# Performance work log

Hardware: AMD Instinct MI355X
Metric: run time of the kernel (lower is better)

Reference implementation:

```python
import jax, jax.numpy as jnp
import numpy as np
import math

N, E, H, NB, NL, NG, NELEM = 50000, 800000, 64, 8, 2, 64, 100
CUTOFF = 5.0


def _lin(k, fin, fout):
    kw, kb = jax.random.split(k)
    bound = 1.0 / math.sqrt(fin)
    w = jax.random.uniform(kw, (fin, fout), jnp.float32, -bound, bound)
    b = jax.random.uniform(kb, (fout,), jnp.float32, -bound, bound)
    return w, b


def setup_inputs() -> dict:
    key = jax.random.key(0)
    ks = jax.random.split(key, 12)
    z = jax.random.randint(ks[0], (N,), 0, NELEM)
    pos = jax.random.normal(ks[1], (N, 3), jnp.float32)
    edge_index = jax.random.randint(ks[2], (2, E), 0, N)
    batch = jnp.sort(jax.random.randint(ks[3], (N,), 0, NG))
    embed = jax.random.normal(ks[4], (NELEM, H), jnp.float32)
    # stacked per-interaction MLP params, leading dim = NL
    msg_w1, msg_b1, msg_w2, msg_b2 = [], [], [], []
    upd_w1, upd_b1, upd_w2, upd_b2 = [], [], [], []
    for l in range(NL):
        kl = jax.random.fold_in(ks[5], l)
        k1, k2, k3, k4 = jax.random.split(kl, 4)
        w, b = _lin(k1, 2 * H + NB, H); msg_w1.append(w); msg_b1.append(b)
        w, b = _lin(k2, H, H); msg_w2.append(w); msg_b2.append(b)
        w, b = _lin(k3, 2 * H, H); upd_w1.append(w); upd_b1.append(b)
        w, b = _lin(k4, H, H); upd_w2.append(w); upd_b2.append(b)
    eh_w1, eh_b1 = _lin(ks[6], H, H)
    eh_w2, eh_b2 = _lin(ks[7], H, 1)
    return {
        "z": z, "pos": pos, "edge_index": edge_index, "batch": batch,
        "embed": embed,
        "msg_w1": jnp.stack(msg_w1), "msg_b1": jnp.stack(msg_b1),
        "msg_w2": jnp.stack(msg_w2), "msg_b2": jnp.stack(msg_b2),
        "upd_w1": jnp.stack(upd_w1), "upd_b1": jnp.stack(upd_b1),
        "upd_w2": jnp.stack(upd_w2), "upd_b2": jnp.stack(upd_b2),
        "eh_w1": eh_w1, "eh_b1": eh_b1, "eh_w2": eh_w2, "eh_b2": eh_b2,
    }


def _mace_energy(pos, embed, msg_w1, msg_b1, msg_w2, msg_b2,
                 upd_w1, upd_b1, upd_w2, upd_b2,
                 eh_w1, eh_b1, eh_w2, eh_b2,
                 z, edge_index, batch):
    row, col = edge_index[0], edge_index[1]
    edge_vec = pos[row] - pos[col]                      # (E,3)
    d = jnp.linalg.norm(edge_vec, axis=-1)              # (E,)
    env = jnp.where(d < CUTOFF,
                    jnp.cos(d * (math.pi / (2 * CUTOFF))) ** 2,
                    0.0)
    freqs = jnp.arange(1, NB + 1, dtype=pos.dtype) * (math.pi / CUTOFF)
    d_safe = jnp.where(d > 0, d, 1.0)[:, None]
    edge_attr = jnp.sin(freqs * d[:, None]) / d_safe * env[:, None]  # (E,NB)

    x = embed[z]                                        # (N,H)
    for l in range(NL):
        # PyG source_to_target: x_j = x[row], x_i = x[col], aggregate at col
        msg_in = jnp.concatenate([x[col], x[row], edge_attr], axis=-1)  # (E,2H+NB)
        m = jax.nn.silu(msg_in @ msg_w1[l] + msg_b1[l]) @ msg_w2[l] + msg_b2[l]
        agg = jax.ops.segment_sum(m, col, num_segments=N)               # (N,H)
        u_in = jnp.concatenate([x, agg], axis=-1)
        upd = jax.nn.silu(u_in @ upd_w1[l] + upd_b1[l]) @ upd_w2[l] + upd_b2[l]
        x = x + upd

    atomic_e = jax.nn.silu(x @ eh_w1 + eh_b1) @ eh_w2 + eh_b2           # (N,1)
    energy = jax.ops.segment_sum(atomic_e, batch, num_segments=NG)      # (NG,1)
    return energy.squeeze(-1)


def reference(z, pos, edge_index, batch, embed,
              msg_w1, msg_b1, msg_w2, msg_b2,
              upd_w1, upd_b1, upd_w2, upd_b2,
              eh_w1, eh_b1, eh_w2, eh_b2):
    return _mace_energy(pos, embed, msg_w1, msg_b1, msg_w2, msg_b2,
                        upd_w1, upd_b1, upd_w2, upd_b2,
                        eh_w1, eh_b1, eh_w2, eh_b2,
                        z, edge_index, batch)
```

## Files before the change

### kernel.cpp

```cpp
#include <hip/hip_runtime.h>
#include <math.h>

#define NN 50000
#define EE 800000
#define HH 64
#define NBASIS 8
#define NLAYER 2
#define NGRAPH 64
#define NBLK1 49

using half2_t = decltype(__builtin_amdgcn_cvt_pkrtz(0.0f, 0.0f));
typedef _Float16 f16x8 __attribute__((ext_vector_type(8)));
typedef float f32x4 __attribute__((ext_vector_type(4)));

union U4H8 { uint4 u; f16x8 h; };

__device__ __forceinline__ float silu_f(float v) {
    return v * (1.0f / (1.0f + __expf(-v)));
}

__device__ __forceinline__ unsigned pk2(float a, float b) {
    union { half2_t h; unsigned u; } x;
    x.h = __builtin_amdgcn_cvt_pkrtz(a, b);
    return x.u;
}

__device__ __forceinline__ half2_t u2h(unsigned u) {
    union { unsigned u; half2_t h; } x; x.u = u; return x.h;
}

__global__ __launch_bounds__(256) void prep_k(
    const int* __restrict__ z, const float* __restrict__ embed,
    unsigned* __restrict__ xh,
    const float* __restrict__ msg_w1, const float* __restrict__ msg_w2,
    const float* __restrict__ upd_w1, const float* __restrict__ upd_w2,
    const float* __restrict__ eh_w1,
    unsigned* __restrict__ w1t, unsigned* __restrict__ w2t,
    unsigned* __restrict__ w1tu, unsigned* __restrict__ w2tu,
    unsigned* __restrict__ ehw1t,
    const int* __restrict__ ecol, int* __restrict__ deg)
{
    int b = blockIdx.x;
    if (b < 6250) {
        int idx = b * 256 + threadIdx.x;
        int n = idx >> 5;
        int p = idx & 31;
        const float2* er = (const float2*)(embed + ((size_t)z[n] << 6));
        float2 v = er[p];
        xh[idx] = pk2(v.x, v.y);
    } else if (b < 6362) {
        int idx = (b - 6250) * 256 + threadIdx.x;
        if (idx < 10240) {
            int l = idx / 5120, rem = idx % 5120;
            int f = rem / 80, kp = rem % 80;
            const float* w = msg_w1 + (size_t)l * 136 * 64;
            unsigned v = 0;
            if (kp < 68) v = pk2(w[(2*kp)*64 + f], w[(2*kp+1)*64 + f]);
            w1t[idx] = v;
        } else if (idx < 14336) {
            int j = idx - 10240;
            int l = j / 2048, rem = j % 2048;
            int n = rem / 32, kp = rem % 32;
            const float* w = msg_w2 + (size_t)l * 64 * 64;
            w2t[j] = pk2(w[(2*kp)*64 + n], w[(2*kp+1)*64 + n]);
        } else if (idx < 22528) {
            int j = idx - 14336;
            int l = j / 4096, rem = j % 4096;
            int f = rem >> 6, kp = rem & 63;
            const float* w = upd_w1 + (size_t)l * 128 * 64;
            w1tu[j] = pk2(w[(2*kp)*64 + f], w[(2*kp+1)*64 + f]);
        } else if (idx < 26624) {
            int j = idx - 22528;
            int l = j / 2048, rem = j % 2048;
            int n = rem / 32, kp = rem % 32;
            const float* w = upd_w2 + (size_t)l * 64 * 64;
            w2tu[j] = pk2(w[(2*kp)*64 + n], w[(2*kp+1)*64 + n]);
        } else if (idx < 28672) {
            int j = idx - 26624;
            int f = j / 32, kp = j % 32;
            ehw1t[j] = pk2(eh_w1[(2*kp)*64 + f], eh_w1[(2*kp+1)*64 + f]);
        }
    } else {
        int e = (b - 6362) * 256 + threadIdx.x;
        if (e < EE) atomicAdd(&deg[ecol[e]], 1);
    }
}

__global__ __launch_bounds__(1024) void scan1_k(
    const int* __restrict__ deg, int* __restrict__ cursor,
    int* __restrict__ bsum)
{
    __shared__ int wsum[16];
    int t = threadIdx.x, lane = t & 63, wave = t >> 6;
    int i = blockIdx.x * 1024 + t;
    int v = (i < NN) ? deg[i] : 0;
    int s = v;
#pragma unroll
    for (int off = 1; off < 64; off <<= 1) {
        int tv = __shfl_up(s, off, 64);
        if (lane >= off) s += tv;
    }
    if (lane == 63) wsum[wave] = s;
    __syncthreads();
    if (wave == 0) {
        int ws = (lane < 16) ? wsum[lane] : 0;
        int ss = ws;
#pragma unroll
        for (int off = 1; off < 16; off <<= 1) {
            int tv = __shfl_up(ss, off, 64);
            if (lane >= off) ss += tv;
        }
        if (lane < 16) wsum[lane] = ss - ws;
    }
    __syncthreads();
    int excl = wsum[wave] + s - v;
    if (i < NN) cursor[i] = excl;
    if (t == 1023) bsum[blockIdx.x] = excl + v;
}

__global__ __launch_bounds__(64) void scan2_k(int* __restrict__ bsum)
{
    int lane = threadIdx.x;
    int v = (lane < NBLK1) ? bsum[lane] : 0;
    int s = v;
#pragma unroll
    for (int off = 1; off < 64; off <<= 1) {
        int tv = __shfl_up(s, off, 64);
        if (lane >= off) s += tv;
    }
    if (lane < NBLK1) bsum[lane] = s - v;
}

__global__ __launch_bounds__(256) void scatter_k(
    const int* __restrict__ erow, const int* __restrict__ ecol,
    const float* __restrict__ pos,
    int* __restrict__ cursor, const int* __restrict__ bsum,
    uint4* __restrict__ edgeS)
{
    int e = blockIdx.x * 256 + threadIdx.x;
    if (e >= EE) return;
    int c = ecol[e], r = erow[e];
    int slot = atomicAdd(&cursor[c], 1) + bsum[c >> 10];
    float dx = pos[3*r]   - pos[3*c];
    float dy = pos[3*r+1] - pos[3*c+1];
    float dz = pos[3*r+2] - pos[3*c+2];
    float d = sqrtf(dx*dx + dy*dy + dz*dz);
    uint4 v;
    v.x = (unsigned)r; v.y = (unsigned)c;
    v.z = __float_as_uint(d); v.w = 0;
    edgeS[slot] = v;
}

__global__ __launch_bounds__(256, 4) void msg_k(
    const uint4* __restrict__ edgeS,
    const unsigned* __restrict__ xh,
    const unsigned* __restrict__ w1t, const float* __restrict__ b1,
    const unsigned* __restrict__ w2t, const float* __restrict__ b2,
    float* __restrict__ agg)
{
    __shared__ __align__(16) unsigned earr[4][64 * 4];
    __shared__ int ckey_s[4][64];
    __shared__ int rkey_s[4][64];
    __shared__ float Mbuf[4][64 * 33];

    const int wid  = threadIdx.x >> 6;
    const int lane = threadIdx.x & 63;
    const int q = lane >> 4, n15 = lane & 15;
    const size_t base = (size_t)blockIdx.x * 256 + wid * 64;

    int mykey;
    {
        uint4 ev = edgeS[base + lane];
        rkey_s[wid][lane] = (int)ev.x;
        mykey = (int)ev.y;
        ckey_s[wid][lane] = mykey;
        float d = __uint_as_float(ev.z);
        float env = 0.0f;
        if (d < 5.0f) {
            float cv = __cosf(d * 0.31415926535897932f);
            env = cv * cv;
        }
        float scale = (d > 0.0f) ? (env / d) : env;
        float ea[NBASIS];
#pragma unroll
        for (int k = 0; k < NBASIS; ++k)
            ea[k] = __sinf((float)(k + 1) * 0.62831853071795865f * d) * scale;
#pragma unroll
        for (int p = 0; p < 4; ++p)
            earr[wid][lane * 4 + p] = pk2(ea[2*p], ea[2*p+1]);
    }
    int pkk = __shfl_up(mykey, 1, 64);
    unsigned long long bmask = __ballot(lane > 0 && mykey != pkk);
    unsigned m32 = (unsigned)(bmask >> (lane & 32));
    __syncthreads();

    int cn[4], rn[4];
#pragma unroll
    for (int nt = 0; nt < 4; ++nt) {
        int eB = nt * 16 + n15;
        cn[nt] = ckey_s[wid][eB];
        rn[nt] = rkey_s[wid][eB];
    }

    f32x4 acc1[4][4];
#pragma unroll
    for (int mt = 0; mt < 4; ++mt) {
        f32x4 binit = *(const f32x4*)(b1 + mt * 16 + q * 4);
#pragma unroll
        for (int nt = 0; nt < 4; ++nt) acc1[mt][nt] = binit;
    }
#pragma unroll
    for (int ks = 0; ks < 5; ++ks) {
        U4H8 bfk[4];
#pragma unroll
        for (int nt = 0; nt < 4; ++nt) {
            if (ks == 4) {
                uint4 zz; zz.x = zz.y = zz.z = zz.w = 0;
                bfk[nt].u = (q == 0) ? *(const uint4*)(earr[wid] + (nt * 16 + n15) * 4) : zz;
            } else if (ks < 2) {
                bfk[nt].u = ((const uint4*)(xh + ((size_t)cn[nt] << 5)))[ks * 4 + q];
            } else {
                bfk[nt].u = ((const uint4*)(xh + ((size_t)rn[nt] << 5)))[(ks - 2) * 4 + q];
            }
        }
#pragma unroll
        for (int mt = 0; mt < 4; ++mt) {
            U4H8 af;
            af.u = *(const uint4*)(w1t + (size_t)(mt * 16 + n15) * 80 + ks * 16 + q * 4);
#pragma unroll
            for (int nt = 0; nt < 4; ++nt)
                acc1[mt][nt] = __builtin_amdgcn_mfma_f32_16x16x32_f16(
                    af.h, bfk[nt].h, acc1[mt][nt], 0, 0, 0);
        }
    }

    unsigned psrc[4][4][2];
#pragma unroll
    for (int mt = 0; mt < 4; ++mt)
#pragma unroll
        for (int nt = 0; nt < 4; ++nt) {
            psrc[mt][nt][0] = pk2(silu_f(acc1[mt][nt][0]), silu_f(acc1[mt][nt][1]));
            psrc[mt][nt][1] = pk2(silu_f(acc1[mt][nt][2]), silu_f(acc1[mt][nt][3]));
        }

    f32x4 acc2[4][4];
#pragma unroll
    for (int nt = 0; nt < 4; ++nt) {
        float b2v = b2[nt * 16 + n15];
        f32x4 binit; binit[0] = b2v; binit[1] = b2v; binit[2] = b2v; binit[3] = b2v;
#pragma unroll
        for (int et = 0; et < 4; ++et) acc2[et][nt] = binit;
    }
#pragma unroll
    for (int ks2 = 0; ks2 < 2; ++ks2) {
        U4H8 wb[4];
#pragma unroll
        for (int nt = 0; nt < 4; ++nt)
            wb[nt].u = *(const uint4*)(w2t + (size_t)(nt * 16 + n15) * 32 + ks2 * 16 + q * 4);
#pragma unroll
        for (int et = 0; et < 4; ++et) {
            unsigned tmp[4];
#pragma unroll
            for (int jr = 0; jr < 4; ++jr) {
                int srcl = (2 * (q & 1) + (jr >> 1)) * 16 + n15;
                unsigned v0 = (unsigned)__shfl((int)psrc[2 * ks2][et][jr & 1], srcl, 64);
                unsigned v1 = (unsigned)__shfl((int)psrc[2 * ks2 + 1][et][jr & 1], srcl, 64);
                tmp[jr] = (q >> 1) ? v1 : v0;
            }
            U4H8 pf;
            pf.u.x = tmp[0]; pf.u.y = tmp[1]; pf.u.z = tmp[2]; pf.u.w = tmp[3];
#pragma unroll
            for (int nt = 0; nt < 4; ++nt)
                acc2[et][nt] = __builtin_amdgcn_mfma_f32_16x16x32_f16(
                    pf.h, wb[nt].h, acc2[et][nt], 0, 0, 0);
        }
    }

#pragma unroll
    for (int hf = 0; hf < 2; ++hf) {
#pragma unroll
        for (int et = 0; et < 4; ++et)
#pragma unroll
            for (int t2 = 0; t2 < 2; ++t2) {
                int nt = 2 * hf + t2;
                int cl = t2 * 16 + n15;
                int eb = et * 16 + q * 4;
#pragma unroll
                for (int r = 0; r < 4; ++r)
                    Mbuf[wid][(eb + r) * 33 + cl] = acc2[et][nt][r];
            }
        __syncthreads();
        {
            int cl = lane & 31, st = lane >> 5;
            int ebase = 32 * st;
            float run = Mbuf[wid][ebase * 33 + cl];
            int runkey = ckey_s[wid][ebase];
            bool atstart = true;
#pragma unroll
            for (int i = 1; i < 32; ++i) {
                float v = Mbuf[wid][(ebase + i) * 33 + cl];
                if ((m32 >> i) & 1u) {
                    float* dst = agg + ((size_t)runkey << 6) + hf * 32 + cl;
                    if (atstart) atomicAdd(dst, run); else *dst = run;
                    runkey = ckey_s[wid][ebase + i]; atstart = false;
                    run = v;
                } else {
                    run += v;
                }
            }
            atomicAdd(agg + ((size_t)runkey << 6) + hf * 32 + cl, run);
        }
        __syncthreads();
    }
}

__global__ __launch_bounds__(256) void upd_k(
    unsigned* __restrict__ xh,
    float* __restrict__ agg,
    const unsigned* __restrict__ w1t, const float* __restrict__ b1,
    const unsigned* __restrict__ w2t, const float* __restrict__ b2,
    const unsigned* __restrict__ ehw1t, const float* __restrict__ ehb1,
    const float* __restrict__ ehw2, const float* __restrict__ ehb2,
    const int* __restrict__ batch, float* __restrict__ energy,
    int do_zero, int do_head)
{
    __shared__ unsigned MU[4][16 * 33];
    __shared__ float esum[NGRAPH];

    const int tid = threadIdx.x;
    const int wid = tid >> 6;
    const int lane = tid & 63;
    const int q = lane >> 4, n15 = lane & 15;
    const int base16 = blockIdx.x * 64 + wid * 16;

    if (do_head) {
        if (tid < NGRAPH) esum[tid] = 0.0f;
        __syncthreads();
    }

    int nodeB = base16 + n15;
    int ncB = (nodeB < NN) ? nodeB : (NN - 1);

    f32x4 acc1[4];
#pragma unroll
    for (int mt = 0; mt < 4; ++mt)
        acc1[mt] = *(const f32x4*)(b1 + mt * 16 + q * 4);
#pragma unroll
    for (int ks = 0; ks < 4; ++ks) {
        U4H8 bfk;
        if (ks < 2) {
            bfk.u = ((const uint4*)(xh + ((size_t)ncB << 5)))[ks * 4 + q];
        } else {
            const float4* ap = (const float4*)(agg + ((size_t)ncB << 6));
            int o = (ks - 2) * 8 + 2 * q;
            float4 a0 = ap[o], a1 = ap[o + 1];
            bfk.u.x = pk2(a0.x, a0.y); bfk.u.y = pk2(a0.z, a0.w);
            bfk.u.z = pk2(a1.x, a1.y); bfk.u.w = pk2(a1.z, a1.w);
        }
#pragma unroll
        for (int mt = 0; mt < 4; ++mt) {
            U4H8 af;
            af.u = *(const uint4*)(w1t + (size_t)(mt * 16 + n15) * 64 + ks * 16 + q * 4);
            acc1[mt] = __builtin_amdgcn_mfma_f32_16x16x32_f16(
                af.h, bfk.h, acc1[mt], 0, 0, 0);
        }
    }

    unsigned psrc[4][2];
#pragma unroll
    for (int mt = 0; mt < 4; ++mt) {
        psrc[mt][0] = pk2(silu_f(acc1[mt][0]), silu_f(acc1[mt][1]));
        psrc[mt][1] = pk2(silu_f(acc1[mt][2]), silu_f(acc1[mt][3]));
    }

    f32x4 acc2[4];
#pragma unroll
    for (int nt = 0; nt < 4; ++nt) {
        float b2v = b2[nt * 16 + n15];
        acc2[nt][0] = b2v; acc2[nt][1] = b2v; acc2[nt][2] = b2v; acc2[nt][3] = b2v;
    }
#pragma unroll
    for (int ks2 = 0; ks2 < 2; ++ks2) {
        unsigned tmp[4];
#pragma unroll
        for (int jr = 0; jr < 4; ++jr) {
            int srcl = (2 * (q & 1) + (jr >> 1)) * 16 + n15;
            unsigned v0 = (unsigned)__shfl((int)psrc[2 * ks2][jr & 1], srcl, 64);
            unsigned v1 = (unsigned)__shfl((int)psrc[2 * ks2 + 1][jr & 1], srcl, 64);
            tmp[jr] = (q >> 1) ? v1 : v0;
        }
        U4H8 pf;
        pf.u.x = tmp[0]; pf.u.y = tmp[1]; pf.u.z = tmp[2]; pf.u.w = tmp[3];
#pragma unroll
        for (int nt = 0; nt < 4; ++nt) {
            U4H8 wb;
            wb.u = *(const uint4*)(w2t + (size_t)(nt * 16 + n15) * 32 + ks2 * 16 + q * 4);
            acc2[nt] = __builtin_amdgcn_mfma_f32_16x16x32_f16(
                pf.h, wb.h, acc2[nt], 0, 0, 0);
        }
    }

#pragma unroll
    for (int nt = 0; nt < 4; ++nt) {
#pragma unroll
        for (int r = 0; r < 4; ++r) {
            int node = base16 + 4 * q + r;
            float vnew = 0.0f;
            if (node < NN) {
                unsigned pu = xh[((size_t)node << 5) + (unsigned)((nt * 16 + n15) >> 1)];
                half2_t hp = u2h(pu);
                float vold = (n15 & 1) ? (float)hp[1] : (float)hp[0];
                vnew = vold + acc2[nt][r];
            }
            float vpart = __shfl_xor(vnew, 1, 64);
            if ((n15 & 1) == 0) {
                unsigned pv = pk2(vnew, vpart);
                int pidx = nt * 8 + (n15 >> 1);
                MU[wid][(4 * q + r) * 33 + pidx] = pv;
                if (node < NN) xh[((size_t)node << 5) + pidx] = pv;
            }
        }
    }

    if (do_zero) {
        if (nodeB < NN) {
            float4 z4; z4.x = z4.y = z4.z = z4.w = 0.0f;
            float4* ap = (float4*)(agg + ((size_t)nodeB << 6));
            ap[2*q] = z4; ap[2*q + 1] = z4;
            ap[8 + 2*q] = z4; ap[8 + 2*q + 1] = z4;
        }
    }

    if (do_head) {
        __syncthreads();
        f32x4 acch[4];
#pragma unroll
        for (int mt = 0; mt < 4; ++mt)
            acch[mt] = *(const f32x4*)(ehb1 + mt * 16 + q * 4);
#pragma unroll
        for (int ks = 0; ks < 2; ++ks) {
            U4H8 bfk;
            bfk.u.x = MU[wid][n15 * 33 + ks * 16 + 4 * q + 0];
            bfk.u.y = MU[wid][n15 * 33 + ks * 16 + 4 * q + 1];
            bfk.u.z = MU[wid][n15 * 33 + ks * 16 + 4 * q + 2];
            bfk.u.w = MU[wid][n15 * 33 + ks * 16 + 4 * q + 3];
#pragma unroll
            for (int mt = 0; mt < 4; ++mt) {
                U4H8 af;
                af.u = *(const uint4*)(ehw1t + (size_t)(mt * 16 + n15) * 32 + ks * 16 + q * 4);
                acch[mt] = __builtin_amdgcn_mfma_f32_16x16x32_f16(
                    af.h, bfk.h, acch[mt], 0, 0, 0);
            }
        }
        f32x4 wv[4];
#pragma unroll
        for (int mt = 0; mt < 4; ++mt)
            wv[mt] = *(const f32x4*)(ehw2 + mt * 16 + q * 4);
        float e = 0.0f;
#pragma unroll
        for (int mt = 0; mt < 4; ++mt)
#pragma unroll
            for (int r = 0; r < 4; ++r)
                e = fmaf(silu_f(acch[mt][r]), wv[mt][r], e);
        e += __shfl_xor(e, 16, 64);
        e += __shfl_xor(e, 32, 64);
        if (q == 0) {
            int node = base16 + n15;
            if (node < NN) atomicAdd(&esum[batch[node]], e + ehb2[0]);
        }
        __syncthreads();
        if (tid < NGRAPH) {
            float v = esum[tid];
            if (v != 0.0f) atomicAdd(energy + tid, v);
        }
    }
}

extern "C" void kernel_launch(void* const* d_in, const int* in_sizes, int n_in,
                              void* d_out, int out_size, void* d_ws, size_t ws_size,
                              hipStream_t stream) {
    const int*   z       = (const int*)  d_in[0];
    const float* pos     = (const float*)d_in[1];
    const int*   eidx    = (const int*)  d_in[2];
    const int*   batch   = (const int*)  d_in[3];
    const float* embed   = (const float*)d_in[4];
    const float* msg_w1  = (const float*)d_in[5];
    const float* msg_b1  = (const float*)d_in[6];
    const float* msg_w2  = (const float*)d_in[7];
    const float* msg_b2  = (const float*)d_in[8];
    const float* upd_w1  = (const float*)d_in[9];
    const float* upd_b1  = (const float*)d_in[10];
    const float* upd_w2  = (const float*)d_in[11];
    const float* upd_b2  = (const float*)d_in[12];
    const float* eh_w1   = (const float*)d_in[13];
    const float* eh_b1   = (const float*)d_in[14];
    const float* eh_w2   = (const float*)d_in[15];
    const float* eh_b2   = (const float*)d_in[16];

    const int* erow = eidx;
    const int* ecol = eidx + EE;

    float*    agg    = (float*)d_ws;
    unsigned* xh     = (unsigned*)(agg + (size_t)NN * HH);
    int*      deg    = (int*)(xh + (size_t)NN * 32);
    int*      cursor = deg + NN;
    int*      bsum   = cursor + NN;
    uint4*    edgeS  = (uint4*)(bsum + 64);
    unsigned* w1t    = (unsigned*)(edgeS + EE);
    unsigned* w2t    = w1t + NLAYER * 64 * 80;
    unsigned* w1tu   = w2t + NLAYER * 64 * 32;
    unsigned* w2tu   = w1tu + NLAYER * 64 * 64;
    unsigned* ehw1t  = w2tu + NLAYER * 64 * 32;
    float*    energy = (float*)d_out;

    (void)hipMemsetAsync(energy, 0, NGRAPH * sizeof(float), stream);
    (void)hipMemsetAsync(deg, 0, NN * sizeof(int), stream);
    (void)hipMemsetAsync(agg, 0, (size_t)NN * HH * sizeof(float), stream);

    prep_k<<<9487, 256, 0, stream>>>(
        z, embed, xh,
        msg_w1, msg_w2, upd_w1, upd_w2, eh_w1,
        w1t, w2t, w1tu, w2tu, ehw1t,
        ecol, deg);

    scan1_k<<<NBLK1, 1024, 0, stream>>>(deg, cursor, bsum);
    scan2_k<<<1, 64, 0, stream>>>(bsum);
    scatter_k<<<(EE + 255) / 256, 256, 0, stream>>>(
        erow, ecol, pos, cursor, bsum, edgeS);

    for (int l = 0; l < NLAYER; ++l) {
        msg_k<<<EE / 256, 256, 0, stream>>>(
            edgeS, xh,
            w1t + (size_t)l * 64 * 80,
            msg_b1 + (size_t)l * HH,
            w2t + (size_t)l * 64 * 32,
            msg_b2 + (size_t)l * HH,
            agg);
        upd_k<<<(NN + 63) / 64, 256, 0, stream>>>(
            xh, agg,
            w1tu + (size_t)l * 64 * 64,
            upd_b1 + (size_t)l * HH,
            w2tu + (size_t)l * 64 * 32,
            upd_b2 + (size_t)l * HH,
            ehw1t, eh_b1, eh_w2, eh_b2, batch, energy,
            (l == 0) ? 1 : 0,
            (l == NLAYER - 1) ? 1 : 0);
    }
}
```

Baseline: 388.4 us.

## Store message aggregation buffer in fp16 with packed half2 atomics and remap blocks

Switches the per-node aggregation buffer from fp32 to fp16. Boundary segments use packed half2 atomic adds, with the other half of the pair set to zero, and interior segments use plain half stores. The update kernel now loads fp16 directly as the MFMA operand with no pack step, and the memset and zeroing traffic is halved. msg_k also remaps block IDs in an 8-way interleave, likely to spread contiguous edge ranges across XCDs. The cost is lower precision in the accumulated sums and half2 atomics that are not native fp32 accumulation, so accuracy may suffer.

```diff
diff --git a/kernel.cpp b/kernel.cpp
--- a/kernel.cpp
+++ b/kernel.cpp
@@ -1,4 +1,5 @@
 #include <hip/hip_runtime.h>
+#include <hip/hip_fp16.h>
 #include <math.h>
 
 #define NN 50000
@@ -156,7 +157,7 @@
     const unsigned* __restrict__ xh,
     const unsigned* __restrict__ w1t, const float* __restrict__ b1,
     const unsigned* __restrict__ w2t, const float* __restrict__ b2,
-    float* __restrict__ agg)
+    __half* __restrict__ agg)
 {
     __shared__ __align__(16) unsigned earr[4][64 * 4];
     __shared__ int ckey_s[4][64];
@@ -166,7 +167,12 @@
     const int wid  = threadIdx.x >> 6;
     const int lane = threadIdx.x & 63;
     const int q = lane >> 4, n15 = lane & 15;
-    const size_t base = (size_t)blockIdx.x * 256 + wid * 64;
+
+    const int NB = EE / 256;
+    const int bcnt = NB >> 3, brem = NB & 7;
+    int xx = blockIdx.x & 7, ii = blockIdx.x >> 3;
+    int bid = xx * bcnt + ((xx < brem) ? xx : brem) + ii;
+    const size_t base = (size_t)bid * 256 + wid * 64;
 
     int mykey;
     {
@@ -292,6 +298,7 @@
         __syncthreads();
         {
             int cl = lane & 31, st = lane >> 5;
+            int col = hf * 32 + cl;
             int ebase = 32 * st;
             float run = Mbuf[wid][ebase * 33 + cl];
             int runkey = ckey_s[wid][ebase];
@@ -300,15 +307,25 @@
             for (int i = 1; i < 32; ++i) {
                 float v = Mbuf[wid][(ebase + i) * 33 + cl];
                 if ((m32 >> i) & 1u) {
-                    float* dst = agg + ((size_t)runkey << 6) + hf * 32 + cl;
-                    if (atstart) atomicAdd(dst, run); else *dst = run;
+                    if (atstart) {
+                        __half2 hv = (col & 1)
+                            ? __floats2half2_rn(0.0f, run)
+                            : __floats2half2_rn(run, 0.0f);
+                        unsafeAtomicAdd(
+                            (__half2*)agg + ((size_t)runkey << 5) + (col >> 1), hv);
+                    } else {
+                        agg[((size_t)runkey << 6) + col] = __float2half(run);
+                    }
                     runkey = ckey_s[wid][ebase + i]; atstart = false;
                     run = v;
                 } else {
                     run += v;
                 }
             }
-            atomicAdd(agg + ((size_t)runkey << 6) + hf * 32 + cl, run);
+            __half2 hv = (col & 1)
+                ? __floats2half2_rn(0.0f, run)
+                : __floats2half2_rn(run, 0.0f);
+            unsafeAtomicAdd((__half2*)agg + ((size_t)runkey << 5) + (col >> 1), hv);
         }
         __syncthreads();
     }
@@ -316,7 +333,7 @@
 
 __global__ __launch_bounds__(256) void upd_k(
     unsigned* __restrict__ xh,
-    float* __restrict__ agg,
+    __half* __restrict__ agg,
     const unsigned* __restrict__ w1t, const float* __restrict__ b1,
     const unsigned* __restrict__ w2t, const float* __restrict__ b2,
     const unsigned* __restrict__ ehw1t, const float* __restrict__ ehb1,
@@ -351,11 +368,7 @@
         if (ks < 2) {
             bfk.u = ((const uint4*)(xh + ((size_t)ncB << 5)))[ks * 4 + q];
         } else {
-            const float4* ap = (const float4*)(agg + ((size_t)ncB << 6));
-            int o = (ks - 2) * 8 + 2 * q;
-            float4 a0 = ap[o], a1 = ap[o + 1];
-            bfk.u.x = pk2(a0.x, a0.y); bfk.u.y = pk2(a0.z, a0.w);
-            bfk.u.z = pk2(a1.x, a1.y); bfk.u.w = pk2(a1.z, a1.w);
+            bfk.u = ((const uint4*)(agg + ((size_t)ncB << 6)))[(ks - 2) * 4 + q];
         }
 #pragma unroll
         for (int mt = 0; mt < 4; ++mt) {
@@ -424,10 +437,9 @@
 
     if (do_zero) {
         if (nodeB < NN) {
-            float4 z4; z4.x = z4.y = z4.z = z4.w = 0.0f;
-            float4* ap = (float4*)(agg + ((size_t)nodeB << 6));
+            uint4 z4; z4.x = z4.y = z4.z = z4.w = 0;
+            uint4* ap = (uint4*)(agg + ((size_t)nodeB << 6));
             ap[2*q] = z4; ap[2*q + 1] = z4;
-            ap[8 + 2*q] = z4; ap[8 + 2*q + 1] = z4;
         }
     }
 
@@ -500,8 +512,8 @@
     const int* erow = eidx;
     const int* ecol = eidx + EE;
 
-    float*    agg    = (float*)d_ws;
-    unsigned* xh     = (unsigned*)(agg + (size_t)NN * HH);
+    float*    aggf   = (float*)d_ws;
+    unsigned* xh     = (unsigned*)(aggf + (size_t)NN * HH);
     int*      deg    = (int*)(xh + (size_t)NN * 32);
     int*      cursor = deg + NN;
     int*      bsum   = cursor + NN;
@@ -511,11 +523,12 @@
     unsigned* w1tu   = w2t + NLAYER * 64 * 32;
     unsigned* w2tu   = w1tu + NLAYER * 64 * 64;
     unsigned* ehw1t  = w2tu + NLAYER * 64 * 32;
+    __half*   agg    = (__half*)aggf;
     float*    energy = (float*)d_out;
 
     (void)hipMemsetAsync(energy, 0, NGRAPH * sizeof(float), stream);
     (void)hipMemsetAsync(deg, 0, NN * sizeof(int), stream);
-    (void)hipMemsetAsync(agg, 0, (size_t)NN * HH * sizeof(float), stream);
+    (void)hipMemsetAsync(agg, 0, (size_t)NN * HH * sizeof(__half), stream);
 
     prep_k<<<9487, 256, 0, stream>>>(
         z, embed, xh,
```

New measurement: 425.8 us. +9.6%, slower.
